# Kernel tuning notes

Measured on AMD Instinct MI355X. Metric: run time of the kernel, lower is better.

Reference implementation:

```python
import jax, jax.numpy as jnp
import numpy as np

DIM = 1024      # feature_size
K = 128         # num_clusters
E = 2           # expansion
G = 8           # groups
ITERN = 3       # Newton-Schulz iterations
DG = E * DIM // G  # 256 per-group dim


def setup_inputs() -> dict:
    key = jax.random.key(0)
    ks = jax.random.split(key, 10)
    f32 = jnp.float32
    return {
        "x": jax.random.normal(ks[0], (32, DIM, 16, 8), dtype=f32),
        "centroids": jax.random.normal(ks[1], (K, DG), dtype=f32) * 0.05,
        "W_inp": jax.random.normal(ks[2], (E * DIM, DIM), dtype=f32) * 0.02,
        "b_inp": jax.random.normal(ks[3], (E * DIM,), dtype=f32) * 0.01,
        "W_g": jax.random.normal(ks[4], (G, E * DIM), dtype=f32) * 0.02,
        "b_g": jax.random.normal(ks[5], (G,), dtype=f32) * 0.01,
        "W_gk": jax.random.normal(ks[6], (G * K, E * DIM), dtype=f32) * 0.02,
        "b_gk": jax.random.normal(ks[7], (G * K,), dtype=f32) * 0.01,
        "W_f": jax.random.normal(ks[8], (1, K), dtype=f32) * 0.05,
        "b_f": jax.random.normal(ks[9], (1,), dtype=f32) * 0.01,
    }


def _covpool(v):
    # v: [bs, d, h, w] -> second-order pooling [bs, d, d]; x @ I_hat @ x^T == centered outer product / M
    bs, d = v.shape[0], v.shape[1]
    m = v.shape[2] * v.shape[3]
    v = v.reshape(bs, d, m)
    vc = v - v.mean(axis=2, keepdims=True)
    return jnp.einsum('bdm,bem->bde', vc, vc) / m


def _sqrtm_ns(cov, iter_n):
    # MPNCOV Newton-Schulz matrix square root (iter_n >= 2)
    d = cov.shape[1]
    I3 = 3.0 * jnp.eye(d, dtype=cov.dtype)[None]
    norm_a = jnp.trace(cov, axis1=1, axis2=2)[:, None, None]  # pre-normalization by trace
    A = cov / norm_a
    ZY = 0.5 * (I3 - A)
    Y = A @ ZY
    Z = ZY
    for _ in range(1, iter_n - 1):
        ZY = 0.5 * (I3 - Z @ Y)
        Y, Z = Y @ ZY, ZY @ Z
    ZY = 0.5 * (Y @ (I3 - Z @ Y))
    return ZY * jnp.sqrt(norm_a)


def _triuvec(cov):
    # row-major upper-triangular (incl. diagonal) vectorization, matching MPNCOV Triuvec
    d = cov.shape[1]
    r, c = np.triu_indices(d)
    return cov[:, r, c]


def reference(x, centroids, W_inp, b_inp, W_g, b_g, W_gk, b_gk, W_f, b_f):
    resolution = x.shape[-1]
    b8, C, H, W = x.shape
    bs = b8 // 8
    # [bs*8, C, H, W] -> [bs, M, N] with M = 8*H*W, N = C
    xt = x.reshape(bs, 8, C, H, W).transpose(0, 2, 1, 3, 4).reshape(bs, C, 8 * H * W)
    xt = jnp.transpose(xt, (0, 2, 1))
    M = xt.shape[1]
    # L2-normalize along feature dim (F.normalize eps clamp)
    xt = xt / jnp.maximum(jnp.linalg.norm(xt, axis=2, keepdims=True), 1e-12)
    h = xt @ W_inp.T + b_inp                               # [bs, M, E*N]
    alpha_g = jax.nn.sigmoid(h @ W_g.T + b_g)              # [bs, M, G]
    alpha_gk = jax.nn.softmax(h @ W_gk.T + b_gk, axis=1)   # NOTE: nn.Softmax(dim=1) -> over M
    alpha_gk = alpha_gk.reshape(bs, M, G, K)
    rx = h.reshape(bs, M, G, DG)                           # [bs, M, G, DG]
    w = alpha_g[..., None] * alpha_gk                      # [bs, M, G, K]
    # fused residual-weighted sum over M: sum_m w*(x - c) = (sum_m w*x) - (sum_m w)*c
    vlad = jnp.einsum('bmgk,bmgd->bgkd', w, rx) - w.sum(axis=1)[..., None] * centroids
    # learnable fusion over clusters K
    vf = jnp.einsum('bgkd,k->bgd', vlad, W_f[0]) + b_f[0]  # [bs, G, DG]
    vf = jnp.transpose(vf, (0, 2, 1))                      # [bs, DG, G]
    vf = vf.reshape(bs, DG, G // resolution, resolution)
    cov = _covpool(vf)
    cov = _sqrtm_ns(cov, ITERN)
    return _triuvec(cov)                                   # [bs, DG*(DG+1)//2]
```

## Files before the change

### kernel.cpp

```cpp
#include <hip/hip_runtime.h>
#include <math.h>

typedef float f32x4 __attribute__((ext_vector_type(4)));
typedef short bf16x8 __attribute__((ext_vector_type(8)));
typedef unsigned short u16;

__device__ __forceinline__ u16 f2bf(float f) {
    unsigned u = __builtin_bit_cast(unsigned, f);
    u += 0x7fff + ((u >> 16) & 1);
    return (u16)(u >> 16);
}
__device__ __forceinline__ float bf2f(u16 s) {
    unsigned v = ((unsigned)s) << 16;
    return __builtin_bit_cast(float, v);
}
__device__ __forceinline__ void gload16(const void* g, void* l) {
    __builtin_amdgcn_global_load_lds(
        (const __attribute__((address_space(1))) unsigned int*)g,
        (__attribute__((address_space(3))) unsigned int*)l, 16, 0, 0);
}

__global__ __launch_bounds__(256) void k_f2bf2(const float* __restrict__ a,
                                               const float* __restrict__ b,
                                               u16* __restrict__ out, int na, int n) {
    int i = (blockIdx.x * 256 + threadIdx.x) * 4;
    if (i < n) {
        const float* src = (i < na) ? (a + i) : (b + (i - na));
        float4 v = *(const float4*)src;
        ushort4 o;
        o.x = f2bf(v.x); o.y = f2bf(v.y); o.z = f2bf(v.z); o.w = f2bf(v.w);
        *(ushort4*)(out + i) = o;
    }
}

__global__ __launch_bounds__(256) void k_transpose_norm(const float* __restrict__ x,
                                                        u16* __restrict__ xtn) {
    int b8 = blockIdx.x;
    int hh = blockIdx.y;
    int tid = threadIdx.x;
    __shared__ float tile[8][1032];
    __shared__ float inv[8];
    const float* src = x + (size_t)b8 * 1024 * 128 + hh * 8;
    #pragma unroll
    for (int r = 0; r < 4; ++r) {
        int c = tid * 4 + r;
        const float* p = src + (size_t)c * 128;
        float4 v0 = *(const float4*)(p);
        float4 v1 = *(const float4*)(p + 4);
        tile[0][c] = v0.x; tile[1][c] = v0.y; tile[2][c] = v0.z; tile[3][c] = v0.w;
        tile[4][c] = v1.x; tile[5][c] = v1.y; tile[6][c] = v1.z; tile[7][c] = v1.w;
    }
    __syncthreads();
    int w = tid >> 5, j = tid & 31;
    float s = 0.f;
    #pragma unroll 8
    for (int i = 0; i < 32; ++i) { float v = tile[w][i * 32 + j]; s += v * v; }
    #pragma unroll
    for (int m = 16; m; m >>= 1) s += __shfl_xor(s, m);
    if (j == 0) inv[w] = 1.0f / fmaxf(sqrtf(s), 1e-12f);
    __syncthreads();
    int b = b8 >> 3, t = b8 & 7;
    int c0 = tid * 4;
    for (int w2 = 0; w2 < 8; ++w2) {
        int m = t * 128 + hh * 8 + w2;
        float sc = inv[w2];
        u16* dst = xtn + ((size_t)b * 1024 + m) * 1024;
        ushort4 o;
        o.x = f2bf(tile[w2][c0 + 0] * sc);
        o.y = f2bf(tile[w2][c0 + 1] * sc);
        o.z = f2bf(tile[w2][c0 + 2] * sc);
        o.w = f2bf(tile[w2][c0 + 3] * sc);
        *(ushort4*)(dst + c0) = o;
    }
}

template <int BM, int BN, int WC, int MODE>
__global__ __launch_bounds__(512) void k_mfma_gemm(
    const u16* __restrict__ A, const u16* __restrict__ B,
    float* __restrict__ Cf, u16* __restrict__ Cb,
    const float* __restrict__ bias, int K, int N)
{
    constexpr int WR = 8 / WC;
    constexpr int WM = BM / WR;
    constexpr int WN = BN / WC;
    constexpr int MR = WM / 16;
    constexpr int NR = WN / 16;
    constexpr int QA = BM / 64;
    constexpr int QB = BN / 64;
    constexpr int S = QA + QB;
    __shared__ u16 As[2][BM * 64];
    __shared__ u16 Bs[2][BN * 64];
    int tid = threadIdx.x, lane = tid & 63, wave = tid >> 6;
    int wr = wave / WC, wc = wave % WC;
    int i0 = blockIdx.y * BM, j0 = blockIdx.x * BN;
    int fr = lane & 15, fg = lane >> 4;
    f32x4 acc[MR][NR] = {};

    int srcOff = ((tid & 7) ^ ((tid >> 3) & 7)) * 8;

    auto stage = [&](int buf, int t) {
        int kt = t * 64;
        #pragma unroll
        for (int q = 0; q < QA; ++q) {
            int row = (q * 512 + tid) >> 3;
            gload16(A + (size_t)(i0 + row) * K + kt + srcOff,
                    &As[buf][(q * 512 + wave * 64) * 8]);
        }
        #pragma unroll
        for (int q = 0; q < QB; ++q) {
            int row = (q * 512 + tid) >> 3;
            gload16(B + (size_t)(j0 + row) * K + kt + srcOff,
                    &Bs[buf][(q * 512 + wave * 64) * 8]);
        }
    };
    auto compute = [&](int buf) {
        #pragma unroll
        for (int h = 0; h < 2; ++h) {
            bf16x8 af[MR], bv[NR];
            #pragma unroll
            for (int mi = 0; mi < MR; ++mi) {
                int row = wr * WM + mi * 16 + fr;
                af[mi] = *(const bf16x8*)&As[buf][row * 64 + ((h * 4 + fg) ^ (fr & 7)) * 8];
            }
            #pragma unroll
            for (int ni = 0; ni < NR; ++ni) {
                int row = wc * WN + ni * 16 + fr;
                bv[ni] = *(const bf16x8*)&Bs[buf][row * 64 + ((h * 4 + fg) ^ (fr & 7)) * 8];
            }
            #pragma unroll
            for (int mi = 0; mi < MR; ++mi)
                #pragma unroll
                for (int ni = 0; ni < NR; ++ni)
                    acc[mi][ni] = __builtin_amdgcn_mfma_f32_16x16x32_bf16(
                        af[mi], bv[ni], acc[mi][ni], 0, 0, 0);
        }
    };

    int nk = K >> 6;
    stage(0, 0);
    int cur = 0;
    for (int t = 0; t < nk; ++t) {
        if (t + 1 < nk) {
            stage(cur ^ 1, t + 1);
            if constexpr (S == 6)       asm volatile("s_waitcnt vmcnt(6)" ::: "memory");
            else if constexpr (S == 4)  asm volatile("s_waitcnt vmcnt(4)" ::: "memory");
            else                        asm volatile("s_waitcnt vmcnt(8)" ::: "memory");
        } else {
            asm volatile("s_waitcnt vmcnt(0)" ::: "memory");
        }
        __builtin_amdgcn_s_barrier();
        __builtin_amdgcn_sched_barrier(0);
        compute(cur);
        __builtin_amdgcn_s_barrier();
        cur ^= 1;
    }

    if (MODE == 1) {
        #pragma unroll
        for (int ni = 0; ni < NR; ++ni) {
            int col = j0 + wc * WN + ni * 16 + fr;
            float bvv = bias[col];
            #pragma unroll
            for (int mi = 0; mi < MR; ++mi)
                #pragma unroll
                for (int r = 0; r < 4; ++r) {
                    int row = i0 + wr * WM + mi * 16 + fg * 4 + r;
                    Cb[(size_t)row * N + col] = f2bf(acc[mi][ni][r] + bvv);
                }
        }
    } else {
        #pragma unroll
        for (int ni = 0; ni < NR; ++ni) {
            int col = j0 + wc * WN + ni * 16 + fr;
            #pragma unroll
            for (int mi = 0; mi < MR; ++mi)
                #pragma unroll
                for (int r = 0; r < 4; ++r) {
                    int row = i0 + wr * WM + mi * 16 + fg * 4 + r;
                    Cf[(size_t)row * N + col] = acc[mi][ni][r];
                }
        }
    }
}

__global__ __launch_bounds__(256) void k_alpha_g(const u16* __restrict__ h,
                                                 const float* __restrict__ Wg,
                                                 const float* __restrict__ bg,
                                                 float* __restrict__ agT) {
    __shared__ float wgl[16384];
    int tid = threadIdx.x;
    #pragma unroll
    for (int i = 0; i < 16; ++i) {
        int idx = tid * 4 + i * 1024;
        *(float4*)&wgl[idx] = *(const float4*)&Wg[idx];
    }
    __syncthreads();
    float bgl[8];
    #pragma unroll
    for (int g = 0; g < 8; ++g) bgl[g] = bg[g];
    int wv = tid >> 6, lane = tid & 63;
    int bm0 = blockIdx.x * 16;
    for (int r = 0; r < 4; ++r) {
        int bm = bm0 + wv * 4 + r;
        const u16* hr = h + (size_t)bm * 2048;
        float acc[8] = {};
        #pragma unroll
        for (int i = 0; i < 4; ++i) {
            int c0 = i * 512 + lane * 8;
            bf16x8 hv8 = *(const bf16x8*)(hr + c0);
            float hf[8];
            #pragma unroll
            for (int j = 0; j < 8; ++j) hf[j] = bf2f((u16)hv8[j]);
            #pragma unroll
            for (int g = 0; g < 8; ++g) {
                const float* wrp = &wgl[g * 2048 + c0];
                #pragma unroll
                for (int j = 0; j < 8; ++j) acc[g] += hf[j] * wrp[j];
            }
        }
        #pragma unroll
        for (int g = 0; g < 8; ++g) {
            #pragma unroll
            for (int off = 32; off; off >>= 1) acc[g] += __shfl_xor(acc[g], off);
        }
        if (lane < 8) {
            int b = bm >> 10, m = bm & 1023;
            agT[((size_t)b * 8 + lane) * 1024 + m] =
                1.f / (1.f + expf(-(acc[lane] + bgl[lane])));
        }
    }
}

__global__ __launch_bounds__(256) void k_softmax(float* __restrict__ lt,
                                                 const float* __restrict__ agT,
                                                 float* __restrict__ wsum) {
    int gk = blockIdx.x, b = blockIdx.y;
    int tid = threadIdx.x;
    float* row = lt + (size_t)gk * 4096 + b * 1024;
    int g = gk >> 7;
    const float* ag = agT + ((size_t)b * 8 + g) * 1024;
    __shared__ float red[4], red2[4], red3[4];
    float4 v = *(const float4*)(row + tid * 4);
    float mx = fmaxf(fmaxf(v.x, v.y), fmaxf(v.z, v.w));
    #pragma unroll
    for (int m = 32; m; m >>= 1) mx = fmaxf(mx, __shfl_xor(mx, m));
    if ((tid & 63) == 0) red[tid >> 6] = mx;
    __syncthreads();
    mx = fmaxf(fmaxf(red[0], red[1]), fmaxf(red[2], red[3]));
    float e0 = expf(v.x - mx), e1 = expf(v.y - mx), e2 = expf(v.z - mx), e3 = expf(v.w - mx);
    float s = e0 + e1 + e2 + e3;
    #pragma unroll
    for (int m = 32; m; m >>= 1) s += __shfl_xor(s, m);
    if ((tid & 63) == 0) red2[tid >> 6] = s;
    __syncthreads();
    s = red2[0] + red2[1] + red2[2] + red2[3];
    float invs = 1.f / s;
    float4 a = *(const float4*)(ag + tid * 4);
    float w0 = e0 * invs * a.x, w1 = e1 * invs * a.y, w2 = e2 * invs * a.z, w3 = e3 * invs * a.w;
    float4 o; o.x = w0; o.y = w1; o.z = w2; o.w = w3;
    *(float4*)(row + tid * 4) = o;
    float t = w0 + w1 + w2 + w3;
    #pragma unroll
    for (int m = 32; m; m >>= 1) t += __shfl_xor(t, m);
    if ((tid & 63) == 0) red3[tid >> 6] = t;
    __syncthreads();
    if (tid == 0) wsum[((size_t)b * 8 + g) * 128 + (gk & 127)] = red3[0] + red3[1] + red3[2] + red3[3];
}

__global__ __launch_bounds__(256) void k_wf_u(const float* __restrict__ wT,
                                              const float* __restrict__ wsum,
                                              const float* __restrict__ Wf,
                                              float* __restrict__ wf, float* __restrict__ u) {
    int ms = blockIdx.x, bg = blockIdx.y;
    int b = bg >> 3, g = bg & 7;
    int tid = threadIdx.x;
    __shared__ float wfl[128];
    __shared__ float part[256];
    if (tid < 128) {
        wfl[tid] = Wf[tid];
        if (ms == 0) u[bg * 128 + tid] = Wf[tid] * wsum[bg * 128 + tid];
    }
    __syncthreads();
    int ml = tid & 127;
    int kh = tid >> 7;
    const float* base = wT + (size_t)(g * 128 + kh * 64) * 4096 + (size_t)b * 1024 + ms * 128;
    float acc = 0.f;
    #pragma unroll 4
    for (int k = 0; k < 64; ++k) acc += wfl[kh * 64 + k] * base[(size_t)k * 4096 + ml];
    part[tid] = acc;
    __syncthreads();
    if (tid < 128) wf[(size_t)bg * 1024 + ms * 128 + ml] = part[tid] + part[tid + 128];
}

__global__ __launch_bounds__(256) void k_vf_partial(const u16* __restrict__ h,
                                                    const float* __restrict__ wf,
                                                    const float* __restrict__ u,
                                                    const float* __restrict__ cent,
                                                    float* __restrict__ vfp) {
    int mc = blockIdx.x;
    int g = blockIdx.y, b = blockIdx.z;
    int d = threadIdx.x;
    __shared__ float wl[64];
    __shared__ float ul[128];
    float acc = 0.f;
    if (mc < 16) {
        if (d < 64) wl[d] = wf[((size_t)b * 8 + g) * 1024 + mc * 64 + d];
        __syncthreads();
        const u16* hb = h + (size_t)b * 1024 * 2048 + (size_t)(mc * 64) * 2048 + g * 256;
        #pragma unroll 4
        for (int m = 0; m < 64; ++m) acc += wl[m] * bf2f(hb[(size_t)m * 2048 + d]);
    } else {
        if (d < 128) ul[d] = u[((size_t)b * 8 + g) * 128 + d];
        __syncthreads();
        for (int k = 0; k < 128; ++k) acc -= ul[k] * cent[k * 256 + d];
    }
    vfp[(((size_t)b * 8 + g) * 17 + mc) * 256 + d] = acc;
}

#define MM8(DST, P, Q) do { if (act) { float s_ = 0.f; \
    _Pragma("unroll") \
    for (int l_ = 0; l_ < 8; ++l_) s_ += P[ii][l_] * Q[l_][jj]; \
    DST[ii][jj] = s_; } __syncthreads(); } while (0)

__global__ __launch_bounds__(256) void k_finalize(const float* __restrict__ vfp,
                                                  const float* __restrict__ bf,
                                                  float* __restrict__ VcOut,
                                                  float* __restrict__ Wrow,
                                                  float* __restrict__ s0) {
    int b = blockIdx.x;
    int tid = threadIdx.x;
    __shared__ float Vl[256][9];
    __shared__ float red[256];
    __shared__ float Sm[8][8], W1[8][8], W2[8][8], YmL[8][8], ZmL[8][8], ZYL[8][8], FmL[8][8];
    int d = tid;
    float bfv = bf[0];
    float vfl[8];
    #pragma unroll
    for (int g = 0; g < 8; ++g) {
        float acc = 0.f;
        for (int mc = 0; mc < 17; ++mc)
            acc += vfp[(((size_t)b * 8 + g) * 17 + mc) * 256 + d];
        vfl[g] = acc + bfv;
    }
    float mean = 0.f;
    #pragma unroll
    for (int g = 0; g < 8; ++g) mean += vfl[g];
    mean *= 0.125f;
    float trp = 0.f;
    #pragma unroll
    for (int g = 0; g < 8; ++g) { float v = vfl[g] - mean; Vl[d][g] = v; trp += v * v; }
    red[tid] = trp;
    __syncthreads();
    for (int s = 128; s > 0; s >>= 1) { if (tid < s) red[tid] += red[tid + s]; __syncthreads(); }
    float tr = red[0] * 0.125f;
    bool act = tid < 64;
    int ii = (tid >> 3) & 7, jj = tid & 7;
    if (act) {
        float sv = 0.f;
        for (int dd = 0; dd < 256; ++dd) sv += Vl[dd][ii] * Vl[dd][jj];
        Sm[ii][jj] = sv / (8.f * tr);
    }
    __syncthreads();
    if (act) {
        YmL[ii][jj] = (ii == jj ? 1.5f : 0.f) - 0.5f * Sm[ii][jj];
        ZmL[ii][jj] = (ii == jj ? -0.5f : 0.f);
    }
    __syncthreads();
    float ya = 0.f, za = 1.5f;
    MM8(W1, Sm, YmL);
    MM8(W2, ZmL, W1);
    float pa = za * ya;
    if (act) ZYL[ii][jj] = -0.5f * (za * YmL[ii][jj] + ya * ZmL[ii][jj] + W2[ii][jj]);
    __syncthreads();
    float zya = 1.5f - 0.5f * pa;
    MM8(W1, Sm, ZYL);
    MM8(W2, YmL, W1);
    if (act) YmL[ii][jj] = ya * ZYL[ii][jj] + zya * YmL[ii][jj] + W2[ii][jj];
    __syncthreads();
    ya = ya * zya;
    MM8(W1, Sm, ZmL);
    MM8(W2, ZYL, W1);
    if (act) ZmL[ii][jj] = zya * ZmL[ii][jj] + za * ZYL[ii][jj] + W2[ii][jj];
    __syncthreads();
    za = zya * za;
    MM8(W1, Sm, YmL);
    MM8(W2, ZmL, W1);
    float p2a = za * ya;
    if (act) ZYL[ii][jj] = za * YmL[ii][jj] + ya * ZmL[ii][jj] + W2[ii][jj];
    __syncthreads();
    MM8(W1, Sm, ZYL);
    MM8(W2, YmL, W1);
    if (act) FmL[ii][jj] = 0.5f * ((3.f - p2a) * YmL[ii][jj] - ya * ZYL[ii][jj] - W2[ii][jj]);
    __syncthreads();
    float fa = 0.5f * ya * (3.f - p2a);
    float sqtr = sqrtf(tr);
    float scaleF = 1.f / (8.f * sqtr);
    #pragma unroll
    for (int jo = 0; jo < 8; ++jo) {
        float sv = 0.f;
        #pragma unroll
        for (int i = 0; i < 8; ++i) sv += Vl[d][i] * FmL[i][jo];
        Wrow[((size_t)b * 256 + d) * 8 + jo] = sv * scaleF;
    }
    #pragma unroll
    for (int jo = 0; jo < 8; ++jo) VcOut[((size_t)b * 256 + d) * 8 + jo] = Vl[d][jo];
    if (tid == 0) s0[b] = fa * sqtr;
}

__global__ __launch_bounds__(256) void k_output(const float* __restrict__ Vc,
                                                const float* __restrict__ Wrow,
                                                const float* __restrict__ s0,
                                                float* __restrict__ out) {
    int dd = blockIdx.x, b = blockIdx.y;
    int e = threadIdx.x;
    __shared__ float Vl[256][9];
    __shared__ float wr[8];
    float4 v0 = *(const float4*)(Vc + ((size_t)b * 256 + e) * 8);
    float4 v1 = *(const float4*)(Vc + ((size_t)b * 256 + e) * 8 + 4);
    Vl[e][0] = v0.x; Vl[e][1] = v0.y; Vl[e][2] = v0.z; Vl[e][3] = v0.w;
    Vl[e][4] = v1.x; Vl[e][5] = v1.y; Vl[e][6] = v1.z; Vl[e][7] = v1.w;
    if (e < 8) wr[e] = Wrow[((size_t)b * 256 + dd) * 8 + e];
    __syncthreads();
    if (e >= dd) {
        float v = (e == dd) ? s0[b] : 0.f;
        #pragma unroll
        for (int j = 0; j < 8; ++j) v += wr[j] * Vl[e][j];
        size_t idx = (size_t)b * 32896 + (size_t)dd * 256 - ((size_t)dd * (dd - 1)) / 2 + (e - dd);
        out[idx] = v;
    }
}

extern "C" void kernel_launch(void* const* d_in, const int* in_sizes, int n_in,
                              void* d_out, int out_size, void* d_ws, size_t ws_size,
                              hipStream_t stream) {
    const float* x    = (const float*)d_in[0];
    const float* cent = (const float*)d_in[1];
    const float* Winp = (const float*)d_in[2];
    const float* binp = (const float*)d_in[3];
    const float* Wg   = (const float*)d_in[4];
    const float* bg   = (const float*)d_in[5];
    const float* Wgk  = (const float*)d_in[6];
    const float* Wf   = (const float*)d_in[8];
    const float* bf   = (const float*)d_in[9];
    float* out = (float*)d_out;
    char* wsb = (char*)d_ws;

    float* lt    = (float*)(wsb);
    u16*   xtnb  = (u16*)(wsb);
    u16*   hb    = (u16*)(wsb + (16ull << 20));
    u16*   winpb = (u16*)(wsb + (32ull << 20));
    u16*   wgkb  = (u16*)(wsb + (36ull << 20));
    float* agT   = (float*)(wsb + (40ull << 20));
    float* wsum  = agT + 32768;
    float* wf    = wsum + 4096;
    float* u     = wf + 32768;
    float* vfp   = u + 4096;
    float* Vc    = vfp + 139264;
    float* Wr    = Vc + 8192;
    float* s0    = Wr + 8192;

    k_transpose_norm<<<dim3(32, 16), 256, 0, stream>>>(x, xtnb);
    k_f2bf2<<<4096, 256, 0, stream>>>(Winp, Wgk, winpb, 2097152, 4194304);
    k_mfma_gemm<256, 128, 2, 1><<<dim3(16, 16), 512, 0, stream>>>(
        xtnb, winpb, nullptr, hb, binp, 1024, 2048);
    k_alpha_g<<<256, 256, 0, stream>>>(hb, Wg, bg, agT);
    k_mfma_gemm<128, 128, 4, 0><<<dim3(32, 8), 512, 0, stream>>>(
        wgkb, hb, lt, nullptr, nullptr, 2048, 4096);
    k_softmax<<<dim3(1024, 4), 256, 0, stream>>>(lt, agT, wsum);
    k_wf_u<<<dim3(8, 32), 256, 0, stream>>>(lt, wsum, Wf, wf, u);
    k_vf_partial<<<dim3(17, 8, 4), 256, 0, stream>>>(hb, wf, u, cent, vfp);
    k_finalize<<<4, 256, 0, stream>>>(vfp, bf, Vc, Wr, s0);
    k_output<<<dim3(256, 4), 256, 0, stream>>>(Vc, Wr, s0, out);
}
```

Measured before the change: 123.9 us.

## Fold input projection into gating weights to skip materializing h

Since h is linear in the normalized input, the projection is folded into the downstream weights. W_gk·W_inp is computed on-device each call with a split-K batched GEMM plus reduction, and W_g·W_inp the same way. The logits GEMM then uses K=1024 directly on the normalized input instead of K=2048 on h, and the VLAD-fusion sum is reassociated as (wf·x)·W_inpᵀ plus bias terms. This removes the 4096x1024x2048 h GEMM and its bf16 storage, at the cost of extra weight-product GEMMs and several small launches, and the rounding changes slightly because the folded weights are cast to bf16.

```diff
diff --git a/kernel.cpp b/kernel.cpp
--- a/kernel.cpp
+++ b/kernel.cpp
@@ -18,19 +18,6 @@
     __builtin_amdgcn_global_load_lds(
         (const __attribute__((address_space(1))) unsigned int*)g,
         (__attribute__((address_space(3))) unsigned int*)l, 16, 0, 0);
-}
-
-__global__ __launch_bounds__(256) void k_f2bf2(const float* __restrict__ a,
-                                               const float* __restrict__ b,
-                                               u16* __restrict__ out, int na, int n) {
-    int i = (blockIdx.x * 256 + threadIdx.x) * 4;
-    if (i < n) {
-        const float* src = (i < na) ? (a + i) : (b + (i - na));
-        float4 v = *(const float4*)src;
-        ushort4 o;
-        o.x = f2bf(v.x); o.y = f2bf(v.y); o.z = f2bf(v.z); o.w = f2bf(v.w);
-        *(ushort4*)(out + i) = o;
-    }
 }
 
 __global__ __launch_bounds__(256) void k_transpose_norm(const float* __restrict__ x,
@@ -74,11 +61,43 @@
     }
 }
 
+__global__ __launch_bounds__(256) void k_prep(const float* __restrict__ Wgk,
+                                              const float* __restrict__ Winp,
+                                              u16* __restrict__ wgkb,
+                                              u16* __restrict__ winpT) {
+    int bid = blockIdx.x, tid = threadIdx.x;
+    if (bid < 2048) {
+        int i = (bid * 256 + tid) * 4;
+        float4 v = *(const float4*)(Wgk + i);
+        ushort4 o;
+        o.x = f2bf(v.x); o.y = f2bf(v.y); o.z = f2bf(v.z); o.w = f2bf(v.w);
+        *(ushort4*)(wgkb + i) = o;
+    } else {
+        int tb = bid - 2048;
+        int er = tb & 31, cr = tb >> 5;
+        __shared__ float tile[64][65];
+        #pragma unroll
+        for (int i = 0; i < 16; ++i) {
+            int idx = tid + i * 256;
+            int r = idx >> 6, c = idx & 63;
+            tile[r][c] = Winp[(size_t)(er * 64 + r) * 1024 + cr * 64 + c];
+        }
+        __syncthreads();
+        #pragma unroll
+        for (int i = 0; i < 16; ++i) {
+            int idx = tid + i * 256;
+            int cc = idx >> 6, rr = idx & 63;
+            winpT[(size_t)(cr * 64 + cc) * 2048 + er * 64 + rr] = f2bf(tile[rr][cc]);
+        }
+    }
+}
+
 template <int BM, int BN, int WC, int MODE>
 __global__ __launch_bounds__(512) void k_mfma_gemm(
     const u16* __restrict__ A, const u16* __restrict__ B,
     float* __restrict__ Cf, u16* __restrict__ Cb,
-    const float* __restrict__ bias, int K, int N)
+    const float* __restrict__ bias, int Kld, int Kloop, int N,
+    long long zA, long long zB, long long zC)
 {
     constexpr int WR = 8 / WC;
     constexpr int WM = BM / WR;
@@ -90,6 +109,8 @@
     constexpr int S = QA + QB;
     __shared__ u16 As[2][BM * 64];
     __shared__ u16 Bs[2][BN * 64];
+    int bz = blockIdx.z;
+    A += (size_t)bz * zA; B += (size_t)bz * zB;
     int tid = threadIdx.x, lane = tid & 63, wave = tid >> 6;
     int wr = wave / WC, wc = wave % WC;
     int i0 = blockIdx.y * BM, j0 = blockIdx.x * BN;
@@ -103,13 +124,13 @@
         #pragma unroll
         for (int q = 0; q < QA; ++q) {
             int row = (q * 512 + tid) >> 3;
-            gload16(A + (size_t)(i0 + row) * K + kt + srcOff,
+            gload16(A + (size_t)(i0 + row) * Kld + kt + srcOff,
                     &As[buf][(q * 512 + wave * 64) * 8]);
         }
         #pragma unroll
         for (int q = 0; q < QB; ++q) {
             int row = (q * 512 + tid) >> 3;
-            gload16(B + (size_t)(j0 + row) * K + kt + srcOff,
+            gload16(B + (size_t)(j0 + row) * Kld + kt + srcOff,
                     &Bs[buf][(q * 512 + wave * 64) * 8]);
         }
     };
@@ -136,7 +157,7 @@
         }
     };
 
-    int nk = K >> 6;
+    int nk = Kloop >> 6;
     stage(0, 0);
     int cur = 0;
     for (int t = 0; t < nk; ++t) {
@@ -169,6 +190,7 @@
                 }
         }
     } else {
+        float* C2 = Cf + (size_t)bz * zC;
         #pragma unroll
         for (int ni = 0; ni < NR; ++ni) {
             int col = j0 + wc * WN + ni * 16 + fr;
@@ -177,57 +199,109 @@
                 #pragma unroll
                 for (int r = 0; r < 4; ++r) {
                     int row = i0 + wr * WM + mi * 16 + fg * 4 + r;
-                    Cf[(size_t)row * N + col] = acc[mi][ni][r];
+                    C2[(size_t)row * N + col] = acc[mi][ni][r];
                 }
         }
     }
 }
 
-__global__ __launch_bounds__(256) void k_alpha_g(const u16* __restrict__ h,
-                                                 const float* __restrict__ Wg,
-                                                 const float* __restrict__ bg,
-                                                 float* __restrict__ agT) {
-    __shared__ float wgl[16384];
+__global__ __launch_bounds__(256) void k_wcred(const float* __restrict__ wcp,
+                                               u16* __restrict__ wcb) {
+    int i = (blockIdx.x * 256 + threadIdx.x) * 4;
+    float4 a = *(const float4*)(wcp + i);
+    float4 b = *(const float4*)(wcp + 1048576 + i);
+    float4 c = *(const float4*)(wcp + 2097152 + i);
+    float4 d = *(const float4*)(wcp + 3145728 + i);
+    ushort4 o;
+    o.x = f2bf(a.x + b.x + c.x + d.x);
+    o.y = f2bf(a.y + b.y + c.y + d.y);
+    o.z = f2bf(a.z + b.z + c.z + d.z);
+    o.w = f2bf(a.w + b.w + c.w + d.w);
+    *(ushort4*)(wcb + i) = o;
+}
+
+__global__ __launch_bounds__(256) void k_wgeff(const float* __restrict__ Winp,
+                                               const float* __restrict__ Wg,
+                                               float* __restrict__ wgp) {
+    int cs = blockIdx.x, es = blockIdx.y;
     int tid = threadIdx.x;
-    #pragma unroll
-    for (int i = 0; i < 16; ++i) {
-        int idx = tid * 4 + i * 1024;
-        *(float4*)&wgl[idx] = *(const float4*)&Wg[idx];
-    }
-    __syncthreads();
-    float bgl[8];
-    #pragma unroll
-    for (int g = 0; g < 8; ++g) bgl[g] = bg[g];
-    int wv = tid >> 6, lane = tid & 63;
-    int bm0 = blockIdx.x * 16;
-    for (int r = 0; r < 4; ++r) {
-        int bm = bm0 + wv * 4 + r;
-        const u16* hr = h + (size_t)bm * 2048;
+    __shared__ float wg_l[8][64];
+    #pragma unroll
+    for (int i = 0; i < 2; ++i) {
+        int idx = tid + i * 256;
+        wg_l[idx >> 6][idx & 63] = Wg[(size_t)(idx >> 6) * 2048 + es * 64 + (idx & 63)];
+    }
+    __syncthreads();
+    int c = cs * 256 + tid;
+    float acc[8] = {};
+    #pragma unroll 4
+    for (int e = 0; e < 64; ++e) {
+        float v = Winp[(size_t)(es * 64 + e) * 1024 + c];
+        #pragma unroll
+        for (int g = 0; g < 8; ++g) acc[g] += wg_l[g][e] * v;
+    }
+    #pragma unroll
+    for (int g = 0; g < 8; ++g) wgp[(size_t)es * 8192 + g * 1024 + c] = acc[g];
+}
+
+__global__ __launch_bounds__(256) void k_wgred(const float* __restrict__ wgp,
+                                               const float* __restrict__ Wg,
+                                               const float* __restrict__ binp,
+                                               const float* __restrict__ bg,
+                                               float* __restrict__ wge,
+                                               float* __restrict__ cg) {
+    int idx = blockIdx.x * 256 + threadIdx.x;
+    float s = 0.f;
+    for (int es = 0; es < 32; ++es) s += wgp[(size_t)es * 8192 + idx];
+    wge[idx] = s;
+    if (blockIdx.x == 0 && threadIdx.x < 8) {
+        float t = bg[threadIdx.x];
+        for (int e = 0; e < 2048; ++e) t += Wg[(size_t)threadIdx.x * 2048 + e] * binp[e];
+        cg[threadIdx.x] = t;
+    }
+}
+
+__global__ __launch_bounds__(256) void k_agT(const u16* __restrict__ xtn,
+                                             const float* __restrict__ wge,
+                                             const float* __restrict__ cg,
+                                             float* __restrict__ agT) {
+    int b = blockIdx.x, ms = blockIdx.y;
+    int tid = threadIdx.x, w = tid >> 6, lane = tid & 63;
+    __shared__ float wgel[8192];
+    __shared__ float cgl[8];
+    #pragma unroll
+    for (int i = 0; i < 8; ++i) {
+        int idx = tid + i * 256;
+        *(float4*)&wgel[idx * 4] = *(const float4*)&wge[idx * 4];
+    }
+    if (tid < 8) cgl[tid] = cg[tid];
+    __syncthreads();
+    for (int r = 0; r < 8; ++r) {
+        int m = ms * 32 + w * 8 + r;
+        const u16* xr = xtn + ((size_t)b * 1024 + m) * 1024;
         float acc[8] = {};
         #pragma unroll
-        for (int i = 0; i < 4; ++i) {
+        for (int i = 0; i < 2; ++i) {
             int c0 = i * 512 + lane * 8;
-            bf16x8 hv8 = *(const bf16x8*)(hr + c0);
-            float hf[8];
-            #pragma unroll
-            for (int j = 0; j < 8; ++j) hf[j] = bf2f((u16)hv8[j]);
+            bf16x8 hv = *(const bf16x8*)(xr + c0);
+            float xf[8];
+            #pragma unroll
+            for (int j = 0; j < 8; ++j) xf[j] = bf2f((u16)hv[j]);
             #pragma unroll
             for (int g = 0; g < 8; ++g) {
-                const float* wrp = &wgl[g * 2048 + c0];
-                #pragma unroll
-                for (int j = 0; j < 8; ++j) acc[g] += hf[j] * wrp[j];
+                float4 wa = *(const float4*)&wgel[g * 1024 + c0];
+                float4 wb = *(const float4*)&wgel[g * 1024 + c0 + 4];
+                acc[g] += xf[0] * wa.x + xf[1] * wa.y + xf[2] * wa.z + xf[3] * wa.w
+                        + xf[4] * wb.x + xf[5] * wb.y + xf[6] * wb.z + xf[7] * wb.w;
             }
         }
         #pragma unroll
-        for (int g = 0; g < 8; ++g) {
+        for (int g = 0; g < 8; ++g)
             #pragma unroll
             for (int off = 32; off; off >>= 1) acc[g] += __shfl_xor(acc[g], off);
-        }
-        if (lane < 8) {
-            int b = bm >> 10, m = bm & 1023;
+        if (lane < 8)
             agT[((size_t)b * 8 + lane) * 1024 + m] =
-                1.f / (1.f + expf(-(acc[lane] + bgl[lane])));
-        }
+                1.f / (1.f + expf(-(acc[lane] + cgl[lane])));
     }
 }
 
@@ -292,29 +366,88 @@
     if (tid < 128) wf[(size_t)bg * 1024 + ms * 128 + ml] = part[tid] + part[tid + 128];
 }
 
-__global__ __launch_bounds__(256) void k_vf_partial(const u16* __restrict__ h,
-                                                    const float* __restrict__ wf,
-                                                    const float* __restrict__ u,
-                                                    const float* __restrict__ cent,
-                                                    float* __restrict__ vfp) {
-    int mc = blockIdx.x;
-    int g = blockIdx.y, b = blockIdx.z;
-    int d = threadIdx.x;
-    __shared__ float wl[64];
-    __shared__ float ul[128];
-    float acc = 0.f;
-    if (mc < 16) {
-        if (d < 64) wl[d] = wf[((size_t)b * 8 + g) * 1024 + mc * 64 + d];
+__global__ __launch_bounds__(256) void k_wfx(const u16* __restrict__ xtn,
+                                             const float* __restrict__ wf,
+                                             float* __restrict__ wfxp) {
+    int cs = blockIdx.x, ms = blockIdx.y, b = blockIdx.z;
+    int tid = threadIdx.x;
+    __shared__ float wfl[8][128];
+    #pragma unroll
+    for (int i = 0; i < 4; ++i) {
+        int idx = tid + i * 256;
+        wfl[idx >> 7][idx & 127] = wf[((size_t)b * 8 + (idx >> 7)) * 1024 + ms * 128 + (idx & 127)];
+    }
+    __syncthreads();
+    int c = cs * 256 + tid;
+    float acc[8] = {};
+    for (int m = 0; m < 128; ++m) {
+        float xv = bf2f(xtn[((size_t)b * 1024 + ms * 128 + m) * 1024 + c]);
+        #pragma unroll
+        for (int g = 0; g < 8; ++g) acc[g] += wfl[g][m] * xv;
+    }
+    #pragma unroll
+    for (int g = 0; g < 8; ++g)
+        wfxp[(((size_t)ms * 4 + b) * 8 + g) * 1024 + c] = acc[g];
+}
+
+__global__ __launch_bounds__(256) void k_vfpart(const float* __restrict__ wfxp,
+                                                const u16* __restrict__ winpT,
+                                                const float* __restrict__ u,
+                                                const float* __restrict__ cent,
+                                                const float* __restrict__ binp,
+                                                float* __restrict__ vfp) {
+    int g = blockIdx.x, cs = blockIdx.y;
+    int tid = threadIdx.x;
+    if (cs < 8) {
+        __shared__ float wfx_l[4][128];
+        #pragma unroll
+        for (int i = 0; i < 2; ++i) {
+            int idx = tid + i * 256;
+            int bb = idx >> 7, c2 = idx & 127;
+            float s = 0.f;
+            #pragma unroll
+            for (int msq = 0; msq < 8; ++msq)
+                s += wfxp[(((size_t)msq * 4 + bb) * 8 + g) * 1024 + cs * 128 + c2];
+            wfx_l[bb][c2] = s;
+        }
         __syncthreads();
-        const u16* hb = h + (size_t)b * 1024 * 2048 + (size_t)(mc * 64) * 2048 + g * 256;
-        #pragma unroll 4
-        for (int m = 0; m < 64; ++m) acc += wl[m] * bf2f(hb[(size_t)m * 2048 + d]);
+        int d = tid;
+        float acc[4] = {};
+        for (int c2 = 0; c2 < 128; ++c2) {
+            float wv = bf2f(winpT[(size_t)(cs * 128 + c2) * 2048 + g * 256 + d]);
+            #pragma unroll
+            for (int bb = 0; bb < 4; ++bb) acc[bb] += wfx_l[bb][c2] * wv;
+        }
+        #pragma unroll
+        for (int bb = 0; bb < 4; ++bb)
+            vfp[(((size_t)bb * 8 + g) * 9 + cs) * 256 + d] = acc[bb];
     } else {
-        if (d < 128) ul[d] = u[((size_t)b * 8 + g) * 128 + d];
+        __shared__ float ul[4][128];
+        __shared__ float swl[4];
+        #pragma unroll
+        for (int i = 0; i < 2; ++i) {
+            int idx = tid + i * 256;
+            ul[idx >> 7][idx & 127] = u[((size_t)(idx >> 7) * 8 + g) * 128 + (idx & 127)];
+        }
         __syncthreads();
-        for (int k = 0; k < 128; ++k) acc -= ul[k] * cent[k * 256 + d];
-    }
-    vfp[(((size_t)b * 8 + g) * 17 + mc) * 256 + d] = acc;
+        if (tid < 4) {
+            float s = 0.f;
+            for (int k = 0; k < 128; ++k) s += ul[tid][k];
+            swl[tid] = s;
+        }
+        __syncthreads();
+        int d = tid;
+        float acc[4] = {};
+        for (int k = 0; k < 128; ++k) {
+            float cv = cent[k * 256 + d];
+            #pragma unroll
+            for (int bb = 0; bb < 4; ++bb) acc[bb] -= ul[bb][k] * cv;
+        }
+        float bi = binp[g * 256 + d];
+        #pragma unroll
+        for (int bb = 0; bb < 4; ++bb)
+            vfp[(((size_t)bb * 8 + g) * 9 + 8) * 256 + d] = acc[bb] + swl[bb] * bi;
+    }
 }
 
 #define MM8(DST, P, Q) do { if (act) { float s_ = 0.f; \
@@ -338,8 +471,8 @@
     #pragma unroll
     for (int g = 0; g < 8; ++g) {
         float acc = 0.f;
-        for (int mc = 0; mc < 17; ++mc)
-            acc += vfp[(((size_t)b * 8 + g) * 17 + mc) * 256 + d];
+        for (int mc = 0; mc < 9; ++mc)
+            acc += vfp[(((size_t)b * 8 + g) * 9 + mc) * 256 + d];
         vfl[g] = acc + bfv;
     }
     float mean = 0.f;
@@ -445,30 +578,40 @@
     float* out = (float*)d_out;
     char* wsb = (char*)d_ws;
 
-    float* lt    = (float*)(wsb);
     u16*   xtnb  = (u16*)(wsb);
-    u16*   hb    = (u16*)(wsb + (16ull << 20));
-    u16*   winpb = (u16*)(wsb + (32ull << 20));
-    u16*   wgkb  = (u16*)(wsb + (36ull << 20));
-    float* agT   = (float*)(wsb + (40ull << 20));
+    float* lt    = (float*)(wsb + (8ull << 20));
+    u16*   wgkb  = (u16*)(wsb + (24ull << 20));
+    u16*   winpT = (u16*)(wsb + (28ull << 20));
+    float* wcp   = (float*)(wsb + (32ull << 20));
+    u16*   wcb   = (u16*)(wsb + (48ull << 20));
+    float* misc  = (float*)(wsb + (50ull << 20));
+    float* wgp   = misc;
+    float* wge   = wgp + 262144;
+    float* cg    = wge + 8192;
+    float* agT   = cg + 8;
     float* wsum  = agT + 32768;
     float* wf    = wsum + 4096;
     float* u     = wf + 32768;
-    float* vfp   = u + 4096;
-    float* Vc    = vfp + 139264;
+    float* wfxp  = u + 4096;
+    float* vfp   = wfxp + 262144;
+    float* Vc    = vfp + 73728;
     float* Wr    = Vc + 8192;
     float* s0    = Wr + 8192;
 
     k_transpose_norm<<<dim3(32, 16), 256, 0, stream>>>(x, xtnb);
-    k_f2bf2<<<4096, 256, 0, stream>>>(Winp, Wgk, winpb, 2097152, 4194304);
-    k_mfma_gemm<256, 128, 2, 1><<<dim3(16, 16), 512, 0, stream>>>(
-        xtnb, winpb, nullptr, hb, binp, 1024, 2048);
-    k_alpha_g<<<256, 256, 0, stream>>>(hb, Wg, bg, agT);
+    k_prep<<<2560, 256, 0, stream>>>(Wgk, Winp, wgkb, winpT);
+    k_wgeff<<<dim3(4, 32), 256, 0, stream>>>(Winp, Wg, wgp);
+    k_wgred<<<32, 256, 0, stream>>>(wgp, Wg, binp, bg, wge, cg);
+    k_mfma_gemm<128, 128, 4, 0><<<dim3(8, 8, 4), 512, 0, stream>>>(
+        wgkb, winpT, wcp, nullptr, nullptr, 2048, 512, 1024, 512LL, 512LL, 1048576LL);
+    k_wcred<<<1024, 256, 0, stream>>>(wcp, wcb);
     k_mfma_gemm<128, 128, 4, 0><<<dim3(32, 8), 512, 0, stream>>>(
-        wgkb, hb, lt, nullptr, nullptr, 2048, 4096);
+        wcb, xtnb, lt, nullptr, nullptr, 1024, 1024, 4096, 0, 0, 0);
+    k_agT<<<dim3(4, 32), 256, 0, stream>>>(xtnb, wge, cg, agT);
     k_softmax<<<dim3(1024, 4), 256, 0, stream>>>(lt, agT, wsum);
     k_wf_u<<<dim3(8, 32), 256, 0, stream>>>(lt, wsum, Wf, wf, u);
-    k_vf_partial<<<dim3(17, 8, 4), 256, 0, stream>>>(hb, wf, u, cent, vfp);
+    k_wfx<<<dim3(4, 8, 4), 256, 0, stream>>>(xtnb, wf, wfxp);
+    k_vfpart<<<dim3(8, 9), 256, 0, stream>>>(wfxp, winpT, u, cent, binp, vfp);
     k_finalize<<<4, 256, 0, stream>>>(vfp, bf, Vc, Wr, s0);
     k_output<<<dim3(256, 4), 256, 0, stream>>>(Vc, Wr, s0, out);
 }
```

After: 168.0 us. 35.6% more time.
